# Kernel optimization log

Hardware: AMD Instinct MI355X
Metric: run time of the kernel (lower is better)

Reference implementation:

```python
import jax, jax.numpy as jnp
import numpy as np

N, E, F, H, L, G, C = 100000, 3200000, 128, 64, 3, 128, 2
BN_EPS = 1e-5


def setup_inputs() -> dict:
    key = jax.random.key(0)
    ks = jax.random.split(key, 16)
    def nrm(k, s, sc=0.05):
        return jax.random.normal(k, s, dtype=jnp.float32) * sc
    return {
        "x": jax.random.normal(ks[0], (N, F), dtype=jnp.float32),
        "lin0_W": nrm(ks[1], (F, H)), "lin0_b": nrm(ks[2], (H,)),
        "eps": jnp.zeros((L,), jnp.float32),                      # GINConv eps per layer
        "W1": nrm(ks[3], (L, H, 2 * H)), "b1": nrm(ks[4], (L, 2 * H)),
        "g1": jnp.ones((L, 2 * H), jnp.float32), "be1": jnp.zeros((L, 2 * H), jnp.float32),
        "W2": nrm(ks[5], (L, 2 * H, H)), "b2": nrm(ks[6], (L, H)),
        "gbn": jnp.ones((L - 1, H), jnp.float32), "bbn": jnp.zeros((L - 1, H), jnp.float32),
        "gate_W": nrm(ks[7], (H, 1)), "gate_b": nrm(ks[8], (1,)),
        "pred_W": nrm(ks[9], (H, H)), "pred_b": nrm(ks[10], (H,)),
        "cls_W": nrm(ks[11], (H, C)), "cls_b": nrm(ks[12], (C,)),
        "edge_index": jax.random.randint(ks[13], (2, E), 0, N),
        "batch": jnp.sort(jax.random.randint(ks[14], (N,), 0, G)),
        "num_graphs": G,
    }


def batchnorm(h, gamma, beta):
    # training-mode BN over node axis, biased variance (torch semantics)
    mu = h.mean(axis=0)
    var = h.var(axis=0)
    return gamma * (h - mu) * jax.lax.rsqrt(var + BN_EPS) + beta


def gin_conv(h, src, dst, eps, W1, b1, g1, be1, W2, b2):
    # message = relu(x_j), aggr='add' at destination
    agg = jax.ops.segment_sum(jax.nn.relu(h[src]), dst, num_segments=h.shape[0])
    z = (1.0 + eps) * h + agg
    z = batchnorm(z @ W1 + b1, g1, be1)          # [N, 2H]
    return jax.nn.relu(z) @ W2 + b2              # [N, H]


def reference(x, lin0_W, lin0_b, eps, W1, b1, g1, be1, W2, b2,
              gbn, bbn, gate_W, gate_b, pred_W, pred_b, cls_W, cls_b,
              edge_index, batch, num_graphs):
    src, dst = edge_index[0], edge_index[1]
    h = x @ lin0_W + lin0_b                      # lin0
    h = gin_conv(h, src, dst, eps[0], W1[0], b1[0], g1[0], be1[0], W2[0], b2[0])
    for i in range(1, L):                        # convs + external BN (not after conv1)
        h = gin_conv(h, src, dst, eps[i], W1[i], b1[i], g1[i], be1[i], W2[i], b2[i])
        h = batchnorm(h, gbn[i - 1], bbn[i - 1])
    # attentional aggregation: segment softmax over gate, weighted sum per graph
    gate = h @ gate_W + gate_b                   # [N, 1]
    gmax = jax.ops.segment_max(gate, batch, num_segments=num_graphs)
    w = jnp.exp(gate - gmax[batch])
    wsum = jax.ops.segment_sum(w, batch, num_segments=num_graphs)
    alpha = w / wsum[batch]                      # [N, 1]
    pooled = jax.ops.segment_sum(alpha * h, batch, num_segments=num_graphs)  # [G, H]
    z = jax.nn.relu(pooled @ pred_W + pred_b)
    return z @ cls_W + cls_b                     # [G, C]
```

## Files before the change

kernel.cpp:

```cpp
#include <hip/hip_runtime.h>
#include <hip/hip_bf16.h>

#define NN 100000
#define EE 3200000
#define HH 64
#define H2 128
#define LL 3
#define GG 128
#define BN_EPSF 1e-5f

#define NBUK 782
#define NBLKC 800
#define CHUNK 4000
#define DMAX 5120

static __device__ __forceinline__ float waveReduceSum64(float v){
  #pragma unroll
  for (int off = 32; off > 0; off >>= 1) v += __shfl_xor(v, off, 64);
  return v;
}

static __device__ __forceinline__ unsigned bf16rne(float f){
  unsigned u = __float_as_uint(f);
  return (u + 0x7FFFu + ((u >> 16) & 1u)) >> 16;
}

static __device__ __forceinline__ void acc16(float* z, uint4 A, uint4 B){
  z[0]  += __uint_as_float(A.x << 16); z[1]  += __uint_as_float(A.x & 0xFFFF0000u);
  z[2]  += __uint_as_float(A.y << 16); z[3]  += __uint_as_float(A.y & 0xFFFF0000u);
  z[4]  += __uint_as_float(A.z << 16); z[5]  += __uint_as_float(A.z & 0xFFFF0000u);
  z[6]  += __uint_as_float(A.w << 16); z[7]  += __uint_as_float(A.w & 0xFFFF0000u);
  z[8]  += __uint_as_float(B.x << 16); z[9]  += __uint_as_float(B.x & 0xFFFF0000u);
  z[10] += __uint_as_float(B.y << 16); z[11] += __uint_as_float(B.y & 0xFFFF0000u);
  z[12] += __uint_as_float(B.z << 16); z[13] += __uint_as_float(B.z & 0xFFFF0000u);
  z[14] += __uint_as_float(B.w << 16); z[15] += __uint_as_float(B.w & 0xFFFF0000u);
}

__global__ __launch_bounds__(256) void kA(const int* __restrict__ dst, int* __restrict__ cntmat){
  __shared__ int hist[NBUK];
  int t = threadIdx.x, blk = blockIdx.x;
  for (int j = t; j < NBUK; j += 256) hist[j] = 0;
  __syncthreads();
  int base = blk * CHUNK;
  for (int i = t; i < CHUNK; i += 256){
    int d = dst[base + i];
    atomicAdd(&hist[d >> 7], 1);
  }
  __syncthreads();
  for (int j = t; j < NBUK; j += 256) cntmat[j * NBLKC + blk] = hist[j];
}

__global__ __launch_bounds__(1024) void kB1(int* __restrict__ cntmat, int* __restrict__ btotal){
  __shared__ int s[1024];
  int t = threadIdx.x, j = blockIdx.x;
  int v = (t < NBLKC) ? cntmat[j * NBLKC + t] : 0;
  s[t] = v; __syncthreads();
  for (int off = 1; off < 1024; off <<= 1){
    int x = (t >= off) ? s[t - off] : 0; __syncthreads();
    s[t] += x; __syncthreads();
  }
  if (t < NBLKC) cntmat[j * NBLKC + t] = s[t] - v;
  if (t == 1023) btotal[j] = s[t];
}

__global__ __launch_bounds__(1024) void kB2(const int* __restrict__ btotal,
                                            int* __restrict__ bucket_start,
                                            int* __restrict__ row_start){
  __shared__ int s[1024];
  int t = threadIdx.x;
  int v = (t < NBUK) ? btotal[t] : 0;
  s[t] = v; __syncthreads();
  for (int off = 1; off < 1024; off <<= 1){
    int x = (t >= off) ? s[t - off] : 0; __syncthreads();
    s[t] += x; __syncthreads();
  }
  if (t < NBUK) bucket_start[t] = s[t] - v;
  if (t == 0){ bucket_start[NBUK] = EE; row_start[NN] = EE; }
}

__global__ __launch_bounds__(256) void kC(const int* __restrict__ src, const int* __restrict__ dst,
                                          const int* __restrict__ cntmat,
                                          const int* __restrict__ bucket_start,
                                          int2* __restrict__ epart){
  __shared__ int off_s[NBUK];
  __shared__ int cur_s[NBUK];
  int t = threadIdx.x, blk = blockIdx.x;
  for (int j = t; j < NBUK; j += 256){
    off_s[j] = bucket_start[j] + cntmat[j * NBLKC + blk];
    cur_s[j] = 0;
  }
  __syncthreads();
  int base = blk * CHUNK;
  for (int i = t; i < CHUNK; i += 256){
    int s0 = src[base + i];
    int d0 = dst[base + i];
    int j = d0 >> 7;
    int loc = atomicAdd(&cur_s[j], 1);
    epart[off_s[j] + loc] = make_int2(s0, d0);
  }
}

__global__ __launch_bounds__(256) void kD(const int2* __restrict__ epart,
                                          const int* __restrict__ bucket_start,
                                          int* __restrict__ row_start, int* __restrict__ elist){
  __shared__ int src_s[DMAX];
  __shared__ short dloc_s[DMAX];
  __shared__ int elist_s[DMAX];
  __shared__ int cnts[128];
  __shared__ int scan_s[128];
  int t = threadIdx.x, b = blockIdx.x;
  int bb = bucket_start[b], be = bucket_start[b + 1];
  int cnt = be - bb;
  int node_base = b << 7;
  if (t < 128) cnts[t] = 0;
  __syncthreads();
  for (int i = t; i < cnt; i += 256){
    int2 p = epart[bb + i];
    src_s[i] = p.x;
    int dl = p.y - node_base;
    dloc_s[i] = (short)dl;
    atomicAdd(&cnts[dl], 1);
  }
  __syncthreads();
  if (t < 128) scan_s[t] = cnts[t];
  __syncthreads();
  for (int off = 1; off < 128; off <<= 1){
    int x = 0;
    if (t < 128 && t >= off) x = scan_s[t - off];
    __syncthreads();
    if (t < 128) scan_s[t] += x;
    __syncthreads();
  }
  if (t < 128){
    int e = scan_s[t] - cnts[t];
    int node = node_base + t;
    if (node < NN) row_start[node] = bb + e;
    cnts[t] = e;
  }
  __syncthreads();
  for (int i = t; i < cnt; i += 256){
    int pos = atomicAdd(&cnts[(int)dloc_s[i]], 1);
    elist_s[pos] = src_s[i];
  }
  __syncthreads();
  for (int i = t; i < cnt; i += 256) elist[bb + i] = elist_s[i];
}

__global__ __launch_bounds__(256, 4) void k_gemm1(const float* __restrict__ h,
                                                  const unsigned short* __restrict__ hb,
                                                  const int* __restrict__ row_start,
                                                  const int* __restrict__ elist,
                                                  const float* __restrict__ W1,
                                                  const float* __restrict__ b1,
                                                  const float* __restrict__ epsArr,
                                                  int layer,
                                                  float* __restrict__ y1,
                                                  double* __restrict__ stats){
  alignas(16) __shared__ float Zs[64 * 64];
  __shared__ float redS[128];
  __shared__ float redQ[128];
  int t = threadIdx.x;
  int R0 = blockIdx.x * 64;
  float epsv = 1.0f + epsArr[layer];
  {
    int r  = t >> 2;
    int kq = (t & 3) * 16;
    int R  = R0 + r;
    float zacc[16];
    if (R < NN){
      const float4* hr = (const float4*)&h[(long long)R * 64 + kq];
      #pragma unroll
      for (int i = 0; i < 4; ++i){
        float4 v = hr[i];
        zacc[4*i+0] = epsv * v.x; zacc[4*i+1] = epsv * v.y;
        zacc[4*i+2] = epsv * v.z; zacc[4*i+3] = epsv * v.w;
      }
      int beg = row_start[R], end = row_start[R + 1];
      int j = beg;
      for (; j + 3 < end; j += 4){
        int s0 = elist[j], s1 = elist[j+1], s2 = elist[j+2], s3 = elist[j+3];
        const uint4* q0 = (const uint4*)(hb + (size_t)s0 * 64 + kq);
        const uint4* q1 = (const uint4*)(hb + (size_t)s1 * 64 + kq);
        const uint4* q2 = (const uint4*)(hb + (size_t)s2 * 64 + kq);
        const uint4* q3 = (const uint4*)(hb + (size_t)s3 * 64 + kq);
        uint4 A0 = q0[0], B0 = q0[1];
        uint4 A1 = q1[0], B1 = q1[1];
        uint4 A2 = q2[0], B2 = q2[1];
        uint4 A3 = q3[0], B3 = q3[1];
        acc16(zacc, A0, B0); acc16(zacc, A1, B1);
        acc16(zacc, A2, B2); acc16(zacc, A3, B3);
      }
      for (; j < end; ++j){
        int s0 = elist[j];
        const uint4* q0 = (const uint4*)(hb + (size_t)s0 * 64 + kq);
        acc16(zacc, q0[0], q0[1]);
      }
    } else {
      #pragma unroll
      for (int i = 0; i < 16; ++i) zacc[i] = 0.f;
    }
    #pragma unroll
    for (int i = 0; i < 16; ++i) Zs[r * 64 + kq + i] = zacc[i];
  }
  __syncthreads();
  int c = t & 31, rg = t >> 5;
  int r0 = rg * 8;
  float a0[8], a1[8], a2[8], a3[8];
  #pragma unroll
  for (int r = 0; r < 8; ++r){ a0[r]=0.f; a1[r]=0.f; a2[r]=0.f; a3[r]=0.f; }
  for (int k4 = 0; k4 < 16; ++k4){
    float w0[4], w1[4], w2[4], w3[4];
    #pragma unroll
    for (int kk = 0; kk < 4; ++kk){
      int k = k4 * 4 + kk;
      w0[kk] = W1[k*128 + c];
      w1[kk] = W1[k*128 + c + 32];
      w2[kk] = W1[k*128 + c + 64];
      w3[kk] = W1[k*128 + c + 96];
    }
    #pragma unroll
    for (int r = 0; r < 8; ++r){
      float4 zv = *(const float4*)&Zs[(r0 + r) * 64 + k4 * 4];
      a0[r] += zv.x*w0[0] + zv.y*w0[1] + zv.z*w0[2] + zv.w*w0[3];
      a1[r] += zv.x*w1[0] + zv.y*w1[1] + zv.z*w1[2] + zv.w*w1[3];
      a2[r] += zv.x*w2[0] + zv.y*w2[1] + zv.z*w2[2] + zv.w*w2[3];
      a3[r] += zv.x*w3[0] + zv.y*w3[1] + zv.z*w3[2] + zv.w*w3[3];
    }
  }
  float b0 = b1[c], bb1 = b1[c+32], bb2 = b1[c+64], bb3 = b1[c+96];
  float s0=0,s1=0,s2=0,s3=0,q0=0,q1=0,q2=0,q3=0;
  #pragma unroll
  for (int r = 0; r < 8; ++r){
    int R = R0 + r0 + r;
    if (R < NN){
      float y0 = a0[r] + b0, yA = a1[r] + bb1, yB = a2[r] + bb2, yC = a3[r] + bb3;
      long long base = (long long)R * 128;
      y1[base + c]      = y0;
      y1[base + c + 32] = yA;
      y1[base + c + 64] = yB;
      y1[base + c + 96] = yC;
      s0 += y0; q0 += y0*y0; s1 += yA; q1 += yA*yA;
      s2 += yB; q2 += yB*yB; s3 += yC; q3 += yC*yC;
    }
  }
  __syncthreads();
  if (t < 128){ redS[t] = 0.f; redQ[t] = 0.f; }
  __syncthreads();
  atomicAdd(&redS[c],      s0); atomicAdd(&redQ[c],      q0);
  atomicAdd(&redS[c + 32], s1); atomicAdd(&redQ[c + 32], q1);
  atomicAdd(&redS[c + 64], s2); atomicAdd(&redQ[c + 64], q2);
  atomicAdd(&redS[c + 96], s3); atomicAdd(&redQ[c + 96], q3);
  __syncthreads();
  if (t < 128){
    atomicAdd(&stats[t],       (double)redS[t]);
    atomicAdd(&stats[128 + t], (double)redQ[t]);
  }
}

__global__ __launch_bounds__(256, 4) void k_gemm_k128(const float* __restrict__ in,
                                                      const float* __restrict__ W,
                                                      const float* __restrict__ b,
                                                      const float* __restrict__ bnp,
                                                      float* __restrict__ out,
                                                      unsigned short* __restrict__ hb,
                                                      double* __restrict__ stats,
                                                      int mode){
  alignas(16) __shared__ float As[64 * 128];
  __shared__ float redS[64];
  __shared__ float redQ[64];
  int t = threadIdx.x;
  int R0 = blockIdx.x * 64;
  {
    const float4* in4 = (const float4*)in;
    float4* As4 = (float4*)As;
    #pragma unroll
    for (int i = 0; i < 8; ++i){
      int idx = t + i * 256;
      int r = idx >> 5;
      int R = R0 + r;
      float4 v = make_float4(0.f, 0.f, 0.f, 0.f);
      if (R < NN){
        v = in4[(long long)R * 32 + (idx & 31)];
        if (mode & 1){
          int k = (idx & 31) * 4;
          v.x = fmaxf(v.x * bnp[k]   + bnp[128 + k],     0.f);
          v.y = fmaxf(v.y * bnp[k+1] + bnp[128 + k + 1], 0.f);
          v.z = fmaxf(v.z * bnp[k+2] + bnp[128 + k + 2], 0.f);
          v.w = fmaxf(v.w * bnp[k+3] + bnp[128 + k + 3], 0.f);
        }
      }
      As4[idx] = v;
    }
  }
  __syncthreads();
  int c = t & 31, rg = t >> 5;
  int r0 = rg * 8;
  float a0[8], a1[8];
  #pragma unroll
  for (int r = 0; r < 8; ++r){ a0[r]=0.f; a1[r]=0.f; }
  for (int k4 = 0; k4 < 32; ++k4){
    float w0[4], w1[4];
    #pragma unroll
    for (int kk = 0; kk < 4; ++kk){
      int k = k4 * 4 + kk;
      w0[kk] = W[k*64 + c];
      w1[kk] = W[k*64 + c + 32];
    }
    #pragma unroll
    for (int r = 0; r < 8; ++r){
      float4 a = *(const float4*)&As[(r0 + r) * 128 + k4 * 4];
      a0[r] += a.x*w0[0] + a.y*w0[1] + a.z*w0[2] + a.w*w0[3];
      a1[r] += a.x*w1[0] + a.y*w1[1] + a.z*w1[2] + a.w*w1[3];
    }
  }
  float b0 = b[c], bA = b[c + 32];
  float s0=0,s1=0,q0=0,q1=0;
  #pragma unroll
  for (int r = 0; r < 8; ++r){
    int R = R0 + r0 + r;
    if (R < NN){
      float y0 = a0[r] + b0, yA = a1[r] + bA;
      long long base = (long long)R * 64;
      out[base + c] = y0;
      out[base + c + 32] = yA;
      hb[base + c]      = (unsigned short)bf16rne(fmaxf(y0, 0.f));
      hb[base + c + 32] = (unsigned short)bf16rne(fmaxf(yA, 0.f));
      s0 += y0; q0 += y0*y0; s1 += yA; q1 += yA*yA;
    }
  }
  if (mode & 2){
    __syncthreads();
    if (t < 64){ redS[t] = 0.f; redQ[t] = 0.f; }
    __syncthreads();
    atomicAdd(&redS[c], s0);      atomicAdd(&redQ[c], q0);
    atomicAdd(&redS[c + 32], s1); atomicAdd(&redQ[c + 32], q1);
    __syncthreads();
    if (t < 64){
      atomicAdd(&stats[t],      (double)redS[t]);
      atomicAdd(&stats[64 + t], (double)redQ[t]);
    }
  }
}

__global__ void k_bnfin(const double* __restrict__ stats, const float* __restrict__ gamma,
                        const float* __restrict__ beta, float* __restrict__ bnp, int C){
  int t = threadIdx.x;
  if (t < C){
    double s = stats[t], q = stats[C + t];
    double mu = s / (double)NN;
    double var = q / (double)NN - mu * mu;
    float rstd = rsqrtf((float)var + BN_EPSF);
    float sc = gamma[t] * rstd;
    bnp[t] = sc;
    bnp[C + t] = beta[t] - (float)mu * sc;
  }
}

__global__ __launch_bounds__(256) void k_affine(float* __restrict__ h, unsigned short* __restrict__ hb,
                                                const float* __restrict__ bnp){
  int i = blockIdx.x * 256 + threadIdx.x;
  float4* h4 = (float4*)h;
  float4 v = h4[i];
  int base = (i * 4) & 63;
  v.x = v.x * bnp[base + 0] + bnp[64 + base + 0];
  v.y = v.y * bnp[base + 1] + bnp[64 + base + 1];
  v.z = v.z * bnp[base + 2] + bnp[64 + base + 2];
  v.w = v.w * bnp[base + 3] + bnp[64 + base + 3];
  h4[i] = v;
  unsigned w0 = bf16rne(fmaxf(v.x, 0.f)) | (bf16rne(fmaxf(v.y, 0.f)) << 16);
  unsigned w1 = bf16rne(fmaxf(v.z, 0.f)) | (bf16rne(fmaxf(v.w, 0.f)) << 16);
  int row = i >> 4;
  *(uint2*)(hb + (size_t)row * 64 + base) = make_uint2(w0, w1);
}

__global__ __launch_bounds__(256) void k_gate(const float* __restrict__ h, const float* __restrict__ gateW,
                                              const float* __restrict__ gateB, const int* __restrict__ batch,
                                              float* __restrict__ gate, unsigned* __restrict__ gmaxkey){
  int lane = threadIdx.x & 63;
  int wid = blockIdx.x * 4 + (threadIdx.x >> 6);
  int nwaves = gridDim.x * 4;
  int chunk = (NN + nwaves - 1) / nwaves;
  int n0 = wid * chunk;
  int n1 = n0 + chunk; if (n1 > NN) n1 = NN;
  if (n0 >= NN) return;
  float gw = gateW[lane];
  float gb = gateB[0];
  int gcur = batch[n0];
  float mcur = -3.402823466e+38f;
  for (int n = n0; n < n1; ++n){
    int g = batch[n];
    if (g != gcur){
      if (lane == 0){
        unsigned u = __float_as_uint(mcur);
        u = (u & 0x80000000u) ? ~u : (u | 0x80000000u);
        atomicMax(&gmaxkey[gcur], u);
      }
      gcur = g;
      mcur = -3.402823466e+38f;
    }
    float v = h[(long long)n * 64 + lane] * gw;
    v = waveReduceSum64(v) + gb;
    if (lane == 0) gate[n] = v;
    mcur = fmaxf(mcur, v);
  }
  if (lane == 0){
    unsigned u = __float_as_uint(mcur);
    u = (u & 0x80000000u) ? ~u : (u | 0x80000000u);
    atomicMax(&gmaxkey[gcur], u);
  }
}

__global__ __launch_bounds__(256) void k_pool(const float* __restrict__ h, const float* __restrict__ gate,
                                              const int* __restrict__ batch, const unsigned* __restrict__ gmaxkey,
                                              float* __restrict__ wsum, float* __restrict__ pooled){
  int lane = threadIdx.x & 63;
  int wid = blockIdx.x * 4 + (threadIdx.x >> 6);
  int nwaves = gridDim.x * 4;
  int chunk = (NN + nwaves - 1) / nwaves;
  int n0 = wid * chunk;
  int n1 = n0 + chunk; if (n1 > NN) n1 = NN;
  if (n0 >= NN) return;
  int gcur = batch[n0];
  unsigned u = gmaxkey[gcur];
  unsigned bits = (u & 0x80000000u) ? (u ^ 0x80000000u) : ~u;
  float m = __uint_as_float(bits);
  float acc = 0.f, wl = 0.f;
  for (int n = n0; n < n1; ++n){
    int g = batch[n];
    if (g != gcur){
      atomicAdd(&pooled[gcur * 64 + lane], acc);
      if (lane == 0) atomicAdd(&wsum[gcur], wl);
      gcur = g;
      u = gmaxkey[g];
      bits = (u & 0x80000000u) ? (u ^ 0x80000000u) : ~u;
      m = __uint_as_float(bits);
      acc = 0.f; wl = 0.f;
    }
    float w = expf(gate[n] - m);
    acc += w * h[(long long)n * 64 + lane];
    wl += w;
  }
  atomicAdd(&pooled[gcur * 64 + lane], acc);
  if (lane == 0) atomicAdd(&wsum[gcur], wl);
}

__global__ __launch_bounds__(64) void k_head(const float* __restrict__ pooled, const float* __restrict__ wsum,
                                             const float* __restrict__ predW, const float* __restrict__ predB,
                                             const float* __restrict__ clsW, const float* __restrict__ clsB,
                                             float* __restrict__ out){
  int g = blockIdx.x, lane = threadIdx.x;
  __shared__ float p[64];
  p[lane] = pooled[g * 64 + lane] / wsum[g];
  __syncthreads();
  float acc = predB[lane];
  for (int i = 0; i < 64; ++i) acc += p[i] * predW[i * 64 + lane];
  float z = fmaxf(acc, 0.f);
  float c0 = z * clsW[lane * 2 + 0];
  float c1 = z * clsW[lane * 2 + 1];
  c0 = waveReduceSum64(c0);
  c1 = waveReduceSum64(c1);
  if (lane == 0){
    out[g * 2 + 0] = c0 + clsB[0];
    out[g * 2 + 1] = c1 + clsB[1];
  }
}

extern "C" void kernel_launch(void* const* d_in, const int* in_sizes, int n_in,
                              void* d_out, int out_size, void* d_ws, size_t ws_size,
                              hipStream_t stream){
  const float* x     = (const float*)d_in[0];
  const float* lin0W = (const float*)d_in[1];
  const float* lin0b = (const float*)d_in[2];
  const float* eps   = (const float*)d_in[3];
  const float* W1    = (const float*)d_in[4];
  const float* b1    = (const float*)d_in[5];
  const float* g1    = (const float*)d_in[6];
  const float* be1   = (const float*)d_in[7];
  const float* W2    = (const float*)d_in[8];
  const float* b2    = (const float*)d_in[9];
  const float* gbn   = (const float*)d_in[10];
  const float* bbn   = (const float*)d_in[11];
  const float* gateW = (const float*)d_in[12];
  const float* gateB = (const float*)d_in[13];
  const float* predW = (const float*)d_in[14];
  const float* predB = (const float*)d_in[15];
  const float* clsW  = (const float*)d_in[16];
  const float* clsB  = (const float*)d_in[17];
  const int* eidx    = (const int*)d_in[18];
  const int* batch   = (const int*)d_in[19];
  const int* src = eidx;
  const int* dst = eidx + EE;
  float* out = (float*)d_out;

  char* ws = (char*)d_ws;
  size_t off = 0;
  auto alloc = [&](size_t bytes) -> char* {
    char* p = ws + off;
    off += (bytes + 15) & ~(size_t)15;
    return p;
  };
  float* h       = (float*)alloc((size_t)NN * 64 * 4);
  float* y1      = (float*)alloc((size_t)NN * 128 * 4);
  int* elist     = (int*)alloc((size_t)EE * 4);
  unsigned short* hb = (unsigned short*)alloc((size_t)NN * 64 * 2);
  int* row_start = (int*)alloc((size_t)(NN + 1) * 4);
  float* gate    = (float*)alloc((size_t)NN * 4);
  double* stats1 = (double*)alloc(256 * 8);
  double* stats2 = (double*)alloc(128 * 8);
  float* bnp1    = (float*)alloc(256 * 4);
  float* bnp2    = (float*)alloc(128 * 4);
  unsigned* gmaxkey = (unsigned*)alloc(128 * 4);
  float* wsum    = (float*)alloc(128 * 4);
  float* pooled  = (float*)alloc(128 * 64 * 4);

  char* ov = (char*)y1;
  int2* epart       = (int2*)ov;
  int*  cntmat      = (int*)(ov + (size_t)EE * 8);
  int*  btotal      = (int*)(ov + (size_t)EE * 8 + (size_t)NBUK * NBLKC * 4);
  int*  bucket_start= (int*)(ov + (size_t)EE * 8 + (size_t)NBUK * NBLKC * 4 + 3136);

  const int GBLK = (NN + 63) / 64;

  kA <<<NBLKC, 256, 0, stream>>>(dst, cntmat);
  kB1<<<NBUK, 1024, 0, stream>>>(cntmat, btotal);
  kB2<<<1, 1024, 0, stream>>>(btotal, bucket_start, row_start);
  kC <<<NBLKC, 256, 0, stream>>>(src, dst, cntmat, bucket_start, epart);
  kD <<<NBUK, 256, 0, stream>>>(epart, bucket_start, row_start, elist);

  k_gemm_k128<<<GBLK, 256, 0, stream>>>(x, lin0W, lin0b, bnp1, h, hb, stats2, 0);

  for (int l = 0; l < LL; ++l){
    hipMemsetAsync(stats1, 0, 256 * 8, stream);
    k_gemm1<<<GBLK, 256, 0, stream>>>(h, hb, row_start, elist, W1 + (size_t)l * 64 * 128,
                                      b1 + l * 128, eps, l, y1, stats1);
    k_bnfin<<<1, 128, 0, stream>>>(stats1, g1 + l * 128, be1 + l * 128, bnp1, 128);
    if (l > 0) hipMemsetAsync(stats2, 0, 128 * 8, stream);
    int mode = 1 | (l > 0 ? 2 : 0);
    k_gemm_k128<<<GBLK, 256, 0, stream>>>(y1, W2 + (size_t)l * 128 * 64, b2 + l * 64,
                                          bnp1, h, hb, stats2, mode);
    if (l > 0){
      k_bnfin<<<1, 64, 0, stream>>>(stats2, gbn + (l - 1) * 64, bbn + (l - 1) * 64, bnp2, 64);
      k_affine<<<(NN * 64 / 4) / 256, 256, 0, stream>>>(h, hb, bnp2);
    }
  }

  hipMemsetAsync(gmaxkey, 0, 128 * 4, stream);
  hipMemsetAsync(wsum, 0, 128 * 4, stream);
  hipMemsetAsync(pooled, 0, 128 * 64 * 4, stream);
  k_gate<<<1024, 256, 0, stream>>>(h, gateW, gateB, batch, gate, gmaxkey);
  k_pool<<<1024, 256, 0, stream>>>(h, gate, batch, gmaxkey, wsum, pooled);
  k_head<<<128, 64, 0, stream>>>(pooled, wsum, predW, predB, clsW, clsB, out);
}
```

Baseline: 898.0 us.

## Store GIN hidden activations in bf16 and pack edge partition entries

The intermediate y1 activation (N x 128) written by the first GEMM is now stored as bf16 instead of fp32, halving its write and read traffic. The second GEMM gets a mode bit that unpacks bf16 to float on load. BN statistics are still accumulated from the fp32 values before rounding. Separately, edge partition entries are packed into a single int (17-bit source plus 7-bit local destination) instead of int2, halving scatter and read traffic in the CSR build, at the cost of bf16 rounding error in y1.

```diff
diff --git a/kernel.cpp b/kernel.cpp
--- a/kernel.cpp
+++ b/kernel.cpp
@@ -81,7 +81,7 @@
 __global__ __launch_bounds__(256) void kC(const int* __restrict__ src, const int* __restrict__ dst,
                                           const int* __restrict__ cntmat,
                                           const int* __restrict__ bucket_start,
-                                          int2* __restrict__ epart){
+                                          int* __restrict__ epart){
   __shared__ int off_s[NBUK];
   __shared__ int cur_s[NBUK];
   int t = threadIdx.x, blk = blockIdx.x;
@@ -96,11 +96,11 @@
     int d0 = dst[base + i];
     int j = d0 >> 7;
     int loc = atomicAdd(&cur_s[j], 1);
-    epart[off_s[j] + loc] = make_int2(s0, d0);
-  }
-}
-
-__global__ __launch_bounds__(256) void kD(const int2* __restrict__ epart,
+    epart[off_s[j] + loc] = s0 | ((d0 & 127) << 17);
+  }
+}
+
+__global__ __launch_bounds__(256) void kD(const int* __restrict__ epart,
                                           const int* __restrict__ bucket_start,
                                           int* __restrict__ row_start, int* __restrict__ elist){
   __shared__ int src_s[DMAX];
@@ -115,9 +115,9 @@
   if (t < 128) cnts[t] = 0;
   __syncthreads();
   for (int i = t; i < cnt; i += 256){
-    int2 p = epart[bb + i];
-    src_s[i] = p.x;
-    int dl = p.y - node_base;
+    int p = epart[bb + i];
+    src_s[i] = p & 0x1FFFF;
+    int dl = p >> 17;
     dloc_s[i] = (short)dl;
     atomicAdd(&cnts[dl], 1);
   }
@@ -154,7 +154,7 @@
                                                   const float* __restrict__ b1,
                                                   const float* __restrict__ epsArr,
                                                   int layer,
-                                                  float* __restrict__ y1,
+                                                  unsigned short* __restrict__ y1b,
                                                   double* __restrict__ stats){
   alignas(16) __shared__ float Zs[64 * 64];
   __shared__ float redS[128];
@@ -234,11 +234,11 @@
     int R = R0 + r0 + r;
     if (R < NN){
       float y0 = a0[r] + b0, yA = a1[r] + bb1, yB = a2[r] + bb2, yC = a3[r] + bb3;
-      long long base = (long long)R * 128;
-      y1[base + c]      = y0;
-      y1[base + c + 32] = yA;
-      y1[base + c + 64] = yB;
-      y1[base + c + 96] = yC;
+      size_t base = (size_t)R * 128;
+      y1b[base + c]      = (unsigned short)bf16rne(y0);
+      y1b[base + c + 32] = (unsigned short)bf16rne(yA);
+      y1b[base + c + 64] = (unsigned short)bf16rne(yB);
+      y1b[base + c + 96] = (unsigned short)bf16rne(yC);
       s0 += y0; q0 += y0*y0; s1 += yA; q1 += yA*yA;
       s2 += yB; q2 += yB*yB; s3 += yC; q3 += yC*yC;
     }
@@ -257,7 +257,7 @@
   }
 }
 
-__global__ __launch_bounds__(256, 4) void k_gemm_k128(const float* __restrict__ in,
+__global__ __launch_bounds__(256, 4) void k_gemm_k128(const void* __restrict__ inRaw,
                                                       const float* __restrict__ W,
                                                       const float* __restrict__ b,
                                                       const float* __restrict__ bnp,
@@ -271,25 +271,32 @@
   int t = threadIdx.x;
   int R0 = blockIdx.x * 64;
   {
-    const float4* in4 = (const float4*)in;
-    float4* As4 = (float4*)As;
     #pragma unroll
     for (int i = 0; i < 8; ++i){
       int idx = t + i * 256;
       int r = idx >> 5;
+      int kk = idx & 31;
       int R = R0 + r;
       float4 v = make_float4(0.f, 0.f, 0.f, 0.f);
       if (R < NN){
-        v = in4[(long long)R * 32 + (idx & 31)];
+        if (mode & 4){
+          uint2 u = ((const uint2*)inRaw)[(size_t)R * 32 + kk];
+          v.x = __uint_as_float(u.x << 16);
+          v.y = __uint_as_float(u.x & 0xFFFF0000u);
+          v.z = __uint_as_float(u.y << 16);
+          v.w = __uint_as_float(u.y & 0xFFFF0000u);
+        } else {
+          v = ((const float4*)inRaw)[(size_t)R * 32 + kk];
+        }
         if (mode & 1){
-          int k = (idx & 31) * 4;
+          int k = kk * 4;
           v.x = fmaxf(v.x * bnp[k]   + bnp[128 + k],     0.f);
           v.y = fmaxf(v.y * bnp[k+1] + bnp[128 + k + 1], 0.f);
           v.z = fmaxf(v.z * bnp[k+2] + bnp[128 + k + 2], 0.f);
           v.w = fmaxf(v.w * bnp[k+3] + bnp[128 + k + 3], 0.f);
         }
       }
-      As4[idx] = v;
+      *(float4*)&As[idx * 4] = v;
     }
   }
   __syncthreads();
@@ -500,7 +507,7 @@
     return p;
   };
   float* h       = (float*)alloc((size_t)NN * 64 * 4);
-  float* y1      = (float*)alloc((size_t)NN * 128 * 4);
+  unsigned short* y1b = (unsigned short*)alloc((size_t)NN * 128 * 2);
   int* elist     = (int*)alloc((size_t)EE * 4);
   unsigned short* hb = (unsigned short*)alloc((size_t)NN * 64 * 2);
   int* row_start = (int*)alloc((size_t)(NN + 1) * 4);
@@ -513,11 +520,11 @@
   float* wsum    = (float*)alloc(128 * 4);
   float* pooled  = (float*)alloc(128 * 64 * 4);
 
-  char* ov = (char*)y1;
-  int2* epart       = (int2*)ov;
-  int*  cntmat      = (int*)(ov + (size_t)EE * 8);
-  int*  btotal      = (int*)(ov + (size_t)EE * 8 + (size_t)NBUK * NBLKC * 4);
-  int*  bucket_start= (int*)(ov + (size_t)EE * 8 + (size_t)NBUK * NBLKC * 4 + 3136);
+  char* ov = (char*)y1b;
+  int*  epart       = (int*)ov;
+  int*  cntmat      = (int*)(ov + (size_t)EE * 4);
+  int*  btotal      = (int*)(ov + (size_t)EE * 4 + (size_t)NBUK * NBLKC * 4);
+  int*  bucket_start= (int*)(ov + (size_t)EE * 4 + (size_t)NBUK * NBLKC * 4 + 3136);
 
   const int GBLK = (NN + 63) / 64;
 
@@ -532,11 +539,11 @@
   for (int l = 0; l < LL; ++l){
     hipMemsetAsync(stats1, 0, 256 * 8, stream);
     k_gemm1<<<GBLK, 256, 0, stream>>>(h, hb, row_start, elist, W1 + (size_t)l * 64 * 128,
-                                      b1 + l * 128, eps, l, y1, stats1);
+                                      b1 + l * 128, eps, l, y1b, stats1);
     k_bnfin<<<1, 128, 0, stream>>>(stats1, g1 + l * 128, be1 + l * 128, bnp1, 128);
     if (l > 0) hipMemsetAsync(stats2, 0, 128 * 8, stream);
-    int mode = 1 | (l > 0 ? 2 : 0);
-    k_gemm_k128<<<GBLK, 256, 0, stream>>>(y1, W2 + (size_t)l * 128 * 64, b2 + l * 64,
+    int mode = 1 | 4 | (l > 0 ? 2 : 0);
+    k_gemm_k128<<<GBLK, 256, 0, stream>>>(y1b, W2 + (size_t)l * 128 * 64, b2 + l * 64,
                                           bnp1, h, hb, stats2, mode);
     if (l > 0){
       k_bnfin<<<1, 64, 0, stream>>>(stats2, gbn + (l - 1) * 64, bbn + (l - 1) * 64, bnp2, 64);
```

New measurement: 877.0 us. 2.3% less time.
